# Kernel optimization log

Measured on AMD Instinct MI355X. Metric: run time of the kernel, lower is better.

The kernel has to match this reference:

```python
import jax, jax.numpy as jnp
import numpy as np

BS, N, C = 1, 50000, 256
H, D = 8, 32            # num_heads, out_dim (per-head)
DEG = 16
E = N * DEG
MIN_FREQ, SCALE = 1.0 / 64, 1.0
ROT_DIM = D // 2        # out_dim // relative_emb_dim = 16


def rotate_half(x):
    x1, x2 = jnp.split(x, 2, axis=-1)
    return jnp.concatenate([-x2, x1], axis=-1)


def apply_rope(t, freqs):
    return t * jnp.cos(freqs) + rotate_half(t) * jnp.sin(freqs)


def rope_freqs(coord):
    # coord: [bs, n] -> freqs [bs, n, ROT_DIM]
    inv_freq = 1.0 / (10000.0 ** (jnp.arange(0, ROT_DIM, 2, dtype=jnp.float32) / ROT_DIM))
    t = coord * (SCALE / MIN_FREQ)
    f = t[..., None] * inv_freq
    return jnp.concatenate([f, f], axis=-1)


def setup_inputs() -> dict:
    key = jax.random.key(0)
    ks = jax.random.split(key, 6)
    h = jax.random.normal(ks[0], (BS, N, C), dtype=jnp.float32)
    pos = jax.random.uniform(ks[1], (BS, N, 2), dtype=jnp.float32)
    Wq = jax.random.normal(ks[2], (C, H * D), dtype=jnp.float32) / np.sqrt(C)
    Wk = jax.random.normal(ks[3], (C, H * D), dtype=jnp.float32) / np.sqrt(C)
    Wv = jax.random.normal(ks[4], (C, H * D), dtype=jnp.float32) / np.sqrt(C)
    src = jax.random.randint(ks[5], (E,), 0, N)
    dst = jnp.repeat(jnp.arange(N), DEG)  # every node receives >=1 edge (no div-by-zero)
    return {"h": h, "pos": pos, "Wq": Wq, "Wk": Wk, "Wv": Wv, "src": src, "dst": dst}


def reference(h, pos, Wq, Wk, Wv, src, dst):
    bs, n, _ = h.shape

    def proj(W):
        return (h @ W).reshape(bs, n, H, D).transpose(0, 2, 1, 3)  # [bs,H,n,D]

    Q, K, V = proj(Wq), proj(Wk), proj(Wv)

    fx = rope_freqs(pos[..., 0])[:, None]  # [bs,1,n,ROT_DIM], broadcast over heads
    fy = rope_freqs(pos[..., 1])[:, None]

    def rope2d(t):
        return jnp.concatenate(
            [apply_rope(t[..., :ROT_DIM], fx), apply_rope(t[..., ROT_DIM:], fy)], axis=-1)

    Q, K = rope2d(Q), rope2d(K)

    # node-first layout [n, bs, H, D] (matches g.ndata)
    Qn = Q.transpose(2, 0, 1, 3)
    Kn = K.transpose(2, 0, 1, 3)
    Vn = V.transpose(2, 0, 1, 3)

    # per-edge score: (K[src] * Q[dst]).sum(-1) / sqrt(D), clamped, exp
    score = jnp.exp(jnp.clip(
        (Kn[src] * Qn[dst]).sum(-1, keepdims=True) / np.sqrt(D), -5.0, 5.0))  # [E,bs,H,1]

    wV = jax.ops.segment_sum(Vn[src] * score, dst, num_segments=n)  # [n,bs,H,D]
    z = jax.ops.segment_sum(score, dst, num_segments=n)             # [n,bs,H,1]

    out = wV / z                                    # [n,bs,H,D]
    return out.transpose(1, 0, 2, 3).reshape(bs, n, H * D)
```

## Files before the change

kernel.cpp:

```cpp
#include <hip/hip_runtime.h>
#include <math.h>
#include <stdint.h>

#define NN   50000
#define NPAD 50048
#define CD   256
#define DEG  16

typedef _Float16 f16;
typedef _Float16 f16x2 __attribute__((ext_vector_type(2)));
typedef _Float16 f16x4 __attribute__((ext_vector_type(4)));
typedef _Float16 f16x8 __attribute__((ext_vector_type(8)));
typedef float    f32x4 __attribute__((ext_vector_type(4)));

typedef const uint32_t __attribute__((address_space(1)))* gptr_t;
typedef uint32_t       __attribute__((address_space(3)))* lptr_t;


__global__ __launch_bounds__(256) void conv_h(const float* __restrict__ h,
                                              f16* __restrict__ o)
{
    size_t i8 = ((size_t)blockIdx.x * 256 + threadIdx.x) * 8;
    if (i8 >= (size_t)NPAD * CD) return;
    f16x8 r;
    if (i8 < (size_t)NN * CD) {
        float4 a = ((const float4*)(h + i8))[0];
        float4 b = ((const float4*)(h + i8))[1];
        r[0] = (f16)a.x; r[1] = (f16)a.y; r[2] = (f16)a.z; r[3] = (f16)a.w;
        r[4] = (f16)b.x; r[5] = (f16)b.y; r[6] = (f16)b.z; r[7] = (f16)b.w;
    } else {
        r = (f16x8)(f16)0.f;
    }
    *(f16x8*)(o + i8) = r;
}

__global__ __launch_bounds__(256) void conv_w(const float* __restrict__ Wq,
                                              const float* __restrict__ Wk,
                                              const float* __restrict__ Wv,
                                              f16* __restrict__ Wt)
{
    const float* W = (blockIdx.y == 0) ? Wq : (blockIdx.y == 1) ? Wk : Wv;
    int n = blockIdx.x, k = threadIdx.x;
    Wt[(size_t)blockIdx.y * 65536 + n * 256 + k] = (f16)W[k * 256 + n];
}

__global__ __launch_bounds__(256) void gemm16(
    const f16* __restrict__ h16, const f16* __restrict__ Wt,
    f16* __restrict__ Qo, f16* __restrict__ Ko, f16* __restrict__ Vo)
{
    __shared__ __align__(16) char lds[32768];

    const int t    = threadIdx.x;
    const int lane = t & 63;
    const int wid  = t >> 6;
    const int tm   = blockIdx.x;
    const int nc0  = blockIdx.y * 128;
    const int z    = blockIdx.z;

    const f16* B = Wt + (size_t)z * 65536;
    f16* O = (z == 0) ? Qo : (z == 1) ? Ko : Vo;

    const int r15 = lane & 15;
    const int g4  = lane >> 4;
    const int l7  = lane & 7;
    const int wm  = (wid >> 1) * 64;
    const int wn  = (wid & 1) * 64;

    f32x4 acc[4][4];
#pragma unroll
    for (int i = 0; i < 4; ++i)
#pragma unroll
        for (int j = 0; j < 4; ++j) acc[i][j] = (f32x4)0.f;

    for (int kb = 0; kb < 4; ++kb) {
#pragma unroll
        for (int i = 0; i < 4; ++i) {
            int L    = i * 256 + t;
            int row  = L >> 3;
            int slot = (L & 7) ^ (row & 7);
            const char* srcA = (const char*)h16 +
                ((size_t)(tm * 128 + row)) * 512 + kb * 128 + slot * 16;
            const char* srcB = (const char*)B +
                ((size_t)(nc0 + row)) * 512 + kb * 128 + slot * 16;
            uint32_t ldsOff = (uint32_t)(i * 256 + (t & 192)) * 16;
            __builtin_amdgcn_global_load_lds((gptr_t)srcA, (lptr_t)(lds + ldsOff), 16, 0, 0);
            __builtin_amdgcn_global_load_lds((gptr_t)srcB, (lptr_t)(lds + 16384 + ldsOff), 16, 0, 0);
        }
        __syncthreads();

#pragma unroll
        for (int ks = 0; ks < 2; ++ks) {
            const int sl = (ks * 4 + g4) ^ l7;
            f16x8 a[4], b[4];
#pragma unroll
            for (int am = 0; am < 4; ++am) {
                int row = wm + am * 16 + r15;
                a[am] = *(const f16x8*)(lds + row * 128 + sl * 16);
            }
#pragma unroll
            for (int bn = 0; bn < 4; ++bn) {
                int row = wn + bn * 16 + r15;
                b[bn] = *(const f16x8*)(lds + 16384 + row * 128 + sl * 16);
            }
#pragma unroll
            for (int am = 0; am < 4; ++am)
#pragma unroll
                for (int bn = 0; bn < 4; ++bn)
                    acc[am][bn] = __builtin_amdgcn_mfma_f32_16x16x32_f16(
                        a[am], b[bn], acc[am][bn], 0, 0, 0);
        }
        if (kb < 3) __syncthreads();
    }

#pragma unroll
    for (int am = 0; am < 4; ++am) {
#pragma unroll
        for (int bn = 0; bn < 4; ++bn) {
            int col = nc0 + wn + bn * 16 + r15;
            int hh  = col >> 5, dd = col & 31;
#pragma unroll
            for (int j = 0; j < 4; ++j) {
                int gm = tm * 128 + wm + am * 16 + g4 * 4 + j;
                if (gm < NN)
                    O[((size_t)hh * NPAD + gm) * 32 + dd] = (f16)acc[am][bn][j];
            }
        }
    }
}

__global__ __launch_bounds__(256) void rope16(const float* __restrict__ pos,
                                              f16* __restrict__ Q,
                                              f16* __restrict__ K)
{
    int n = blockIdx.x * 256 + threadIdx.x;
    if (n >= NN) return;
    int hd = blockIdx.y;

    float cx = pos[2 * n] * 64.f;
    float cy = pos[2 * n + 1] * 64.f;
    size_t base = ((size_t)hd * NPAD + n) * 32;

    union U { f16 h[32]; float4 v[4]; } q, k;
#pragma unroll
    for (int i = 0; i < 4; ++i) {
        q.v[i] = ((const float4*)(Q + base))[i];
        k.v[i] = ((const float4*)(K + base))[i];
    }

    const float INVF[8] = {1.f, 0.31622776601683794f, 0.1f, 0.031622776601683794f,
                           0.01f, 0.0031622776601683794f, 0.001f, 0.00031622776601683794f};
#pragma unroll
    for (int j = 0; j < 8; ++j) {
        float sx, cxs, sy, cys;
        __sincosf(cx * INVF[j], &sx, &cxs);
        __sincosf(cy * INVF[j], &sy, &cys);
        float a, b;
        a = (float)q.h[j];      b = (float)q.h[j + 8];
        q.h[j] = (f16)(a * cxs - b * sx);  q.h[j + 8] = (f16)(b * cxs + a * sx);
        a = (float)k.h[j];      b = (float)k.h[j + 8];
        k.h[j] = (f16)(a * cxs - b * sx);  k.h[j + 8] = (f16)(b * cxs + a * sx);
        a = (float)q.h[16 + j]; b = (float)q.h[24 + j];
        q.h[16 + j] = (f16)(a * cys - b * sy);  q.h[24 + j] = (f16)(b * cys + a * sy);
        a = (float)k.h[16 + j]; b = (float)k.h[24 + j];
        k.h[16 + j] = (f16)(a * cys - b * sy);  k.h[24 + j] = (f16)(b * cys + a * sy);
    }

#pragma unroll
    for (int i = 0; i < 4; ++i) {
        ((float4*)(Q + base))[i] = q.v[i];
        ((float4*)(K + base))[i] = k.v[i];
    }
}

__global__ __launch_bounds__(256) void scoreK(
    const f16* __restrict__ Q, const f16* __restrict__ K,
    const int* __restrict__ src, float* __restrict__ scores)
{
    const int tid = threadIdx.x;
    const int h   = blockIdx.y;
    const int n   = blockIdx.x * 4 + (tid >> 6);
    const int l   = tid & 63;
    const int j   = l >> 2;
    const int p   = l & 3;

    const int s = src[n * DEG + j];

    f16x8 q8 = *(const f16x8*)(Q + ((size_t)h * NPAD + n) * 32 + p * 8);
    f16x8 k8 = *(const f16x8*)(K + ((size_t)h * NPAD + s) * 32 + p * 8);

    const f16x2* qp = (const f16x2*)&q8;
    const f16x2* kp = (const f16x2*)&k8;
    float d = 0.f;
#if __has_builtin(__builtin_amdgcn_fdot2)
    d = __builtin_amdgcn_fdot2(qp[0], kp[0], d, false);
    d = __builtin_amdgcn_fdot2(qp[1], kp[1], d, false);
    d = __builtin_amdgcn_fdot2(qp[2], kp[2], d, false);
    d = __builtin_amdgcn_fdot2(qp[3], kp[3], d, false);
#else
#pragma unroll
    for (int u = 0; u < 4; ++u)
        d += (float)qp[u].x * (float)kp[u].x + (float)qp[u].y * (float)kp[u].y;
#endif

    d += __shfl_xor(d, 1);
    d += __shfl_xor(d, 2);

    if (p == 0)
        scores[((size_t)h * NN + n) * DEG + j] =
            __expf(fminf(fmaxf(d * 0.17677669529663687f, -5.f), 5.f));
}

__global__ __launch_bounds__(256) void aggV(
    const f16* __restrict__ V, const int* __restrict__ src,
    const float* __restrict__ scores, float* __restrict__ out)
{
    const int tid = threadIdx.x;
    const int h   = blockIdx.y;
    const int g   = blockIdx.x * 256 + tid;
    const int n   = g >> 3;
    const int ln  = g & 7;
    if (n >= NN) return;

    const float4* S4 = (const float4*)(scores + ((size_t)h * NN + n) * DEG);
    float4 s0 = S4[0], s1 = S4[1], s2 = S4[2], s3 = S4[3];
    float w[16] = {s0.x, s0.y, s0.z, s0.w, s1.x, s1.y, s1.z, s1.w,
                   s2.x, s2.y, s2.z, s2.w, s3.x, s3.y, s3.z, s3.w};

    const int4* SR = (const int4*)(src + n * DEG);
    int4 r0 = SR[0], r1 = SR[1], r2 = SR[2], r3 = SR[3];
    int sj[16] = {r0.x, r0.y, r0.z, r0.w, r1.x, r1.y, r1.z, r1.w,
                  r2.x, r2.y, r2.z, r2.w, r3.x, r3.y, r3.z, r3.w};

    float z = 0.f;
#pragma unroll
    for (int j = 0; j < DEG; ++j) z += w[j];

    float a0 = 0.f, a1 = 0.f, a2 = 0.f, a3 = 0.f;
#pragma unroll
    for (int j = 0; j < DEG; ++j) {
        f16x4 v4 = *(const f16x4*)(V + ((size_t)h * NPAD + sj[j]) * 32 + ln * 4);
        a0 += w[j] * (float)v4[0];
        a1 += w[j] * (float)v4[1];
        a2 += w[j] * (float)v4[2];
        a3 += w[j] * (float)v4[3];
    }
    float rz = 1.f / z;
    float4 o;
    o.x = a0 * rz; o.y = a1 * rz; o.z = a2 * rz; o.w = a3 * rz;
    *(float4*)(out + (size_t)n * CD + h * 32 + ln * 4) = o;
}

extern "C" void kernel_launch(void* const* d_in, const int* in_sizes, int n_in,
                              void* d_out, int out_size, void* d_ws, size_t ws_size,
                              hipStream_t stream)
{
    const float* h   = (const float*)d_in[0];
    const float* pos = (const float*)d_in[1];
    const float* Wq  = (const float*)d_in[2];
    const float* Wk  = (const float*)d_in[3];
    const float* Wv  = (const float*)d_in[4];
    const int*   src = (const int*)d_in[5];
    float* out = (float*)d_out;

    char* w = (char*)d_ws;
    f16*   h16    = (f16*)w;
    float* scores = (float*)w;
    f16*   Wt     = (f16*)(w + 25624576);
    f16*   Qb     = (f16*)(w + 26017792);
    f16*   Kb     = (f16*)(w + 51642368);
    f16*   Vb     = (f16*)(w + 77266944);

    conv_h<<<(NPAD * CD / 8 + 255) / 256, 256, 0, stream>>>(h, h16);
    conv_w<<<dim3(256, 3), 256, 0, stream>>>(Wq, Wk, Wv, Wt);
    gemm16<<<dim3(391, 2, 3), 256, 0, stream>>>(h16, Wt, Qb, Kb, Vb);
    rope16<<<dim3((NN + 255) / 256, 8), 256, 0, stream>>>(pos, Qb, Kb);
    scoreK<<<dim3(12500, 8), 256, 0, stream>>>(Qb, Kb, src, scores);
    aggV<<<dim3(1563, 8), 256, 0, stream>>>(Vb, src, scores, out);
}
```

Measured before the change: 292.0 us.

## Fuse RoPE into GEMM epilogue, merge conversion kernels, interleave head blocks

Moves the 2D rotary embedding into the GEMM epilogue. The pair element is fetched with a lane shuffle (xor 8) and sin/cos are computed per row from pos, which removes the separate rope pass that re-read and re-wrote Q and K. It also merges the h and W fp16 conversions into one launch. The score and aggregation grids are flattened so that the 8 heads of a node group sit in adjacent blocks, which should improve cache reuse of src and the gathered rows. The cost is extra sincos work and shuffles in the GEMM epilogue, which is repeated per column tile.

```diff
diff --git a/kernel.cpp b/kernel.cpp
--- a/kernel.cpp
+++ b/kernel.cpp
@@ -17,35 +17,41 @@
 typedef uint32_t       __attribute__((address_space(3)))* lptr_t;
 
 
-__global__ __launch_bounds__(256) void conv_h(const float* __restrict__ h,
-                                              f16* __restrict__ o)
-{
-    size_t i8 = ((size_t)blockIdx.x * 256 + threadIdx.x) * 8;
-    if (i8 >= (size_t)NPAD * CD) return;
-    f16x8 r;
-    if (i8 < (size_t)NN * CD) {
-        float4 a = ((const float4*)(h + i8))[0];
-        float4 b = ((const float4*)(h + i8))[1];
-        r[0] = (f16)a.x; r[1] = (f16)a.y; r[2] = (f16)a.z; r[3] = (f16)a.w;
-        r[4] = (f16)b.x; r[5] = (f16)b.y; r[6] = (f16)b.z; r[7] = (f16)b.w;
+#define CONVH_BLOCKS 6256
+
+__global__ __launch_bounds__(256) void conv_hw(
+    const float* __restrict__ h,
+    const float* __restrict__ Wq, const float* __restrict__ Wk,
+    const float* __restrict__ Wv,
+    f16* __restrict__ o, f16* __restrict__ Wt)
+{
+    int b = blockIdx.x;
+    if (b < CONVH_BLOCKS) {
+        size_t i8 = ((size_t)b * 256 + threadIdx.x) * 8;
+        if (i8 >= (size_t)NPAD * CD) return;
+        f16x8 r;
+        if (i8 < (size_t)NN * CD) {
+            float4 a = ((const float4*)(h + i8))[0];
+            float4 c = ((const float4*)(h + i8))[1];
+            r[0] = (f16)a.x; r[1] = (f16)a.y; r[2] = (f16)a.z; r[3] = (f16)a.w;
+            r[4] = (f16)c.x; r[5] = (f16)c.y; r[6] = (f16)c.z; r[7] = (f16)c.w;
+        } else {
+            r = (f16x8)(f16)0.f;
+        }
+        *(f16x8*)(o + i8) = r;
     } else {
-        r = (f16x8)(f16)0.f;
-    }
-    *(f16x8*)(o + i8) = r;
-}
-
-__global__ __launch_bounds__(256) void conv_w(const float* __restrict__ Wq,
-                                              const float* __restrict__ Wk,
-                                              const float* __restrict__ Wv,
-                                              f16* __restrict__ Wt)
-{
-    const float* W = (blockIdx.y == 0) ? Wq : (blockIdx.y == 1) ? Wk : Wv;
-    int n = blockIdx.x, k = threadIdx.x;
-    Wt[(size_t)blockIdx.y * 65536 + n * 256 + k] = (f16)W[k * 256 + n];
+        int bb = b - CONVH_BLOCKS;
+        int m  = bb >> 8;
+        int n  = bb & 255;
+        const float* W = (m == 0) ? Wq : (m == 1) ? Wk : Wv;
+        int k = threadIdx.x;
+        Wt[(size_t)m * 65536 + n * 256 + k] = (f16)W[k * 256 + n];
+    }
 }
 
 __global__ __launch_bounds__(256) void gemm16(
     const f16* __restrict__ h16, const f16* __restrict__ Wt,
+    const float* __restrict__ pos,
     f16* __restrict__ Qo, f16* __restrict__ Ko, f16* __restrict__ Vo)
 {
     __shared__ __align__(16) char lds[32768];
@@ -112,63 +118,53 @@
         if (kb < 3) __syncthreads();
     }
 
+    const float INVF[8] = {1.f, 0.31622776601683794f, 0.1f, 0.031622776601683794f,
+                           0.01f, 0.0031622776601683794f, 0.001f, 0.00031622776601683794f};
+    const float invf = INVF[l7] * 64.f;
+    const bool  hi   = (r15 & 8) != 0;
+
 #pragma unroll
     for (int am = 0; am < 4; ++am) {
-#pragma unroll
-        for (int bn = 0; bn < 4; ++bn) {
-            int col = nc0 + wn + bn * 16 + r15;
-            int hh  = col >> 5, dd = col & 31;
+        if (z < 2) {
+            float sx[4], cx[4], sy[4], cy[4];
 #pragma unroll
             for (int j = 0; j < 4; ++j) {
                 int gm = tm * 128 + wm + am * 16 + g4 * 4 + j;
-                if (gm < NN)
-                    O[((size_t)hh * NPAD + gm) * 32 + dd] = (f16)acc[am][bn][j];
-            }
-        }
-    }
-}
-
-__global__ __launch_bounds__(256) void rope16(const float* __restrict__ pos,
-                                              f16* __restrict__ Q,
-                                              f16* __restrict__ K)
-{
-    int n = blockIdx.x * 256 + threadIdx.x;
-    if (n >= NN) return;
-    int hd = blockIdx.y;
-
-    float cx = pos[2 * n] * 64.f;
-    float cy = pos[2 * n + 1] * 64.f;
-    size_t base = ((size_t)hd * NPAD + n) * 32;
-
-    union U { f16 h[32]; float4 v[4]; } q, k;
-#pragma unroll
-    for (int i = 0; i < 4; ++i) {
-        q.v[i] = ((const float4*)(Q + base))[i];
-        k.v[i] = ((const float4*)(K + base))[i];
-    }
-
-    const float INVF[8] = {1.f, 0.31622776601683794f, 0.1f, 0.031622776601683794f,
-                           0.01f, 0.0031622776601683794f, 0.001f, 0.00031622776601683794f};
-#pragma unroll
-    for (int j = 0; j < 8; ++j) {
-        float sx, cxs, sy, cys;
-        __sincosf(cx * INVF[j], &sx, &cxs);
-        __sincosf(cy * INVF[j], &sy, &cys);
-        float a, b;
-        a = (float)q.h[j];      b = (float)q.h[j + 8];
-        q.h[j] = (f16)(a * cxs - b * sx);  q.h[j + 8] = (f16)(b * cxs + a * sx);
-        a = (float)k.h[j];      b = (float)k.h[j + 8];
-        k.h[j] = (f16)(a * cxs - b * sx);  k.h[j + 8] = (f16)(b * cxs + a * sx);
-        a = (float)q.h[16 + j]; b = (float)q.h[24 + j];
-        q.h[16 + j] = (f16)(a * cys - b * sy);  q.h[24 + j] = (f16)(b * cys + a * sy);
-        a = (float)k.h[16 + j]; b = (float)k.h[24 + j];
-        k.h[16 + j] = (f16)(a * cys - b * sy);  k.h[24 + j] = (f16)(b * cys + a * sy);
-    }
-
-#pragma unroll
-    for (int i = 0; i < 4; ++i) {
-        ((float4*)(Q + base))[i] = q.v[i];
-        ((float4*)(K + base))[i] = k.v[i];
+                int gc = (gm < NN) ? gm : 0;
+                float2 p = *(const float2*)(pos + 2 * gc);
+                __sincosf(p.x * invf, &sx[j], &cx[j]);
+                __sincosf(p.y * invf, &sy[j], &cy[j]);
+            }
+#pragma unroll
+            for (int bn = 0; bn < 4; ++bn) {
+                int col = nc0 + wn + bn * 16 + r15;
+                int hh  = col >> 5, dd = col & 31;
+                const bool yhalf = (dd & 16) != 0;
+#pragma unroll
+                for (int j = 0; j < 4; ++j) {
+                    float v    = acc[am][bn][j];
+                    float part = __shfl_xor(v, 8);
+                    float c = yhalf ? cy[j] : cx[j];
+                    float s = yhalf ? sy[j] : sx[j];
+                    float res = hi ? (v * c + part * s) : (v * c - part * s);
+                    int gm = tm * 128 + wm + am * 16 + g4 * 4 + j;
+                    if (gm < NN)
+                        O[((size_t)hh * NPAD + gm) * 32 + dd] = (f16)res;
+                }
+            }
+        } else {
+#pragma unroll
+            for (int bn = 0; bn < 4; ++bn) {
+                int col = nc0 + wn + bn * 16 + r15;
+                int hh  = col >> 5, dd = col & 31;
+#pragma unroll
+                for (int j = 0; j < 4; ++j) {
+                    int gm = tm * 128 + wm + am * 16 + g4 * 4 + j;
+                    if (gm < NN)
+                        O[((size_t)hh * NPAD + gm) * 32 + dd] = (f16)acc[am][bn][j];
+                }
+            }
+        }
     }
 }
 
@@ -176,10 +172,10 @@
     const f16* __restrict__ Q, const f16* __restrict__ K,
     const int* __restrict__ src, float* __restrict__ scores)
 {
-    const int tid = threadIdx.x;
-    const int h   = blockIdx.y;
-    const int n   = blockIdx.x * 4 + (tid >> 6);
-    const int l   = tid & 63;
+    const int b   = blockIdx.x;
+    const int h   = b & 7;
+    const int n   = (b >> 3) * 4 + (threadIdx.x >> 6);
+    const int l   = threadIdx.x & 63;
     const int j   = l >> 2;
     const int p   = l & 3;
 
@@ -214,9 +210,9 @@
     const f16* __restrict__ V, const int* __restrict__ src,
     const float* __restrict__ scores, float* __restrict__ out)
 {
-    const int tid = threadIdx.x;
-    const int h   = blockIdx.y;
-    const int g   = blockIdx.x * 256 + tid;
+    const int b   = blockIdx.x;
+    const int h   = b & 7;
+    const int g   = (b >> 3) * 256 + threadIdx.x;
     const int n   = g >> 3;
     const int ln  = g & 7;
     if (n >= NN) return;
@@ -270,10 +266,8 @@
     f16*   Kb     = (f16*)(w + 51642368);
     f16*   Vb     = (f16*)(w + 77266944);
 
-    conv_h<<<(NPAD * CD / 8 + 255) / 256, 256, 0, stream>>>(h, h16);
-    conv_w<<<dim3(256, 3), 256, 0, stream>>>(Wq, Wk, Wv, Wt);
-    gemm16<<<dim3(391, 2, 3), 256, 0, stream>>>(h16, Wt, Qb, Kb, Vb);
-    rope16<<<dim3((NN + 255) / 256, 8), 256, 0, stream>>>(pos, Qb, Kb);
-    scoreK<<<dim3(12500, 8), 256, 0, stream>>>(Qb, Kb, src, scores);
-    aggV<<<dim3(1563, 8), 256, 0, stream>>>(Vb, src, scores, out);
-}
+    conv_hw<<<CONVH_BLOCKS + 768, 256, 0, stream>>>(h, Wq, Wk, Wv, h16, Wt);
+    gemm16<<<dim3(391, 2, 3), 256, 0, stream>>>(h16, Wt, pos, Qb, Kb, Vb);
+    scoreK<<<100000, 256, 0, stream>>>(Qb, Kb, src, scores);
+    aggV<<<12504, 256, 0, stream>>>(Vb, src, scores, out);
+}
```

After: 267.5 us. 8.4% less time.
